# Kernel optimization log

Measured on AMD Instinct MI355X. Metric: run time of the kernel, lower is better.

Reference implementation:

```python
import jax, jax.numpy as jnp
from jax import lax
import numpy as np

D_IN, D, H, W, POOL = 1280, 100, 20, 3, 9
K_SIG, X0 = 1.0, 0.0
EPS = 1e-5


def setup_inputs() -> dict:
    key = jax.random.key(0)
    ks = jax.random.split(key, 8)
    N1, N2 = 512, 512
    return {
        "x1": jax.random.normal(ks[0], (N1, D_IN), jnp.float32),
        "x2": jax.random.normal(ks[1], (N2, D_IN), jnp.float32),
        "W1": jax.random.normal(ks[2], (D, D_IN), jnp.float32) * 0.02,
        "b1": jnp.zeros((D,), jnp.float32),
        "W2": jax.random.normal(ks[3], (H, 2 * D), jnp.float32) * 0.05,
        "b2": jnp.zeros((H,), jnp.float32),
        "bn1_g": jnp.ones((H,), jnp.float32),
        "bn1_b": jnp.zeros((H,), jnp.float32),
        "conv_w": jax.random.normal(ks[4], (1, H, 2 * W + 1, 2 * W + 1), jnp.float32) * 0.05,
        "conv_b": jnp.zeros((1,), jnp.float32),
        "bn2_g": jnp.ones((1,), jnp.float32),
        "bn2_b": jnp.zeros((1,), jnp.float32),
        "gamma": jnp.zeros((1,), jnp.float32),
    }


def reference(x1, x2, W1, b1, W2, b2, bn1_g, bn1_b, conv_w, conv_b, bn2_g, bn2_b, gamma):
    N1, N2 = x1.shape[0], x2.shape[0]
    # fc1 projection (relu1/dropout1 are defined but unused in the original forward)
    a = (x1 @ W1.T + b1)[None]          # [1, N1, D]
    c = (x2 @ W1.T + b2 * 0 + b1)[None] if False else (x2 @ W1.T + b1)[None]  # [1, N2, D]
    # broadcast pairwise |diff| and product -> [1, N1, N2, 2D]
    diff = jnp.abs(a[:, :, None, :] - c[:, None, :, :])
    mul = a[:, :, None, :] * c[:, None, :, :]
    m = jnp.concatenate([diff, mul], axis=-1).reshape(-1, 2 * D)  # [N1*N2, 2D]
    # fc2
    m = m @ W2.T + b2                    # [N1*N2, H]
    # BatchNorm1d in training mode: batch statistics, biased variance
    mu = m.mean(axis=0)
    var = m.var(axis=0)
    m = (m - mu) * lax.rsqrt(var + EPS) * bn1_g + bn1_b
    m = jax.nn.relu(m)
    m = m.reshape(1, N1, N2, H).transpose(0, 3, 1, 2)  # NCHW [1, H, N1, N2]
    # 7x7 conv, padding=W
    C = lax.conv_general_dilated(m, conv_w, (1, 1), [(W, W), (W, W)])
    C = C + conv_b.reshape(1, -1, 1, 1)
    # BatchNorm2d (training mode, biased variance over N,H,W per channel)
    mu2 = C.mean(axis=(0, 2, 3), keepdims=True)
    var2 = C.var(axis=(0, 2, 3), keepdims=True)
    C = (C - mu2) * lax.rsqrt(var2 + EPS) * bn2_g.reshape(1, -1, 1, 1) + bn2_b.reshape(1, -1, 1, 1)
    C = jax.nn.sigmoid(C)
    # MaxPool2d(9, padding=4): stride = kernel, -inf padding
    p = POOL // 2
    B = lax.reduce_window(C, -jnp.inf, lax.max, (1, 1, POOL, POOL), (1, 1, POOL, POOL),
                          [(0, 0), (0, 0), (p, p), (p, p)])
    # mean / unbiased std over dims (1, 2) keepdim
    mean = B.mean(axis=(1, 2), keepdims=True)
    std = jnp.sqrt(B.var(axis=(1, 2), keepdims=True, ddof=1) + EPS)
    Q = jax.nn.relu(B - mean - gamma.reshape(()) * std)
    phat = Q.sum() / (jnp.sign(Q).sum() + 1.0)
    phat = jnp.clip(jax.nn.sigmoid(K_SIG * (phat - X0)), 0.0, 1.0)
    return phat, C
```

## Files before the change

### kernel.cpp

```cpp
#include <hip/hip_runtime.h>
#include <hip/hip_bf16.h>
#include <math.h>

#define N1 512
#define N2 512
#define DIN 1280
#define DD 100
#define HH 20
#define NPIX (N1*N2)
#define PB 57

typedef short bf16x8 __attribute__((ext_vector_type(8)));
typedef float f32x4 __attribute__((ext_vector_type(4)));

static constexpr size_t WS_PP    = 0;
static constexpr size_t WS_W1T   = 204800;
static constexpr size_t WS_W2B   = 332800;
static constexpr size_t WS_M     = 336896;
static constexpr size_t WS_PART  = WS_M + 5242880;
static constexpr size_t WS_CRAW  = WS_PART + 1310720;
static constexpr size_t WS_STATS = WS_CRAW + 262144;
static constexpr size_t WS_B     = WS_STATS + 64;

__global__ __launch_bounds__(256) void kP(const float* __restrict__ W1,
                                          const float* __restrict__ W2,
                                          float* __restrict__ w1t,
                                          unsigned short* __restrict__ w2b,
                                          float* __restrict__ stats) {
  const int tid = threadIdx.x;
  if (blockIdx.x >= 160) {
    int idx = (blockIdx.x - 160) * 256 + tid;
    if (blockIdx.x == 160 && tid < 64) stats[tid] = 0.0f;
    if (idx < 224 * 32) {
      int k = idx >> 5, n = idx & 31;
      float v = (n < HH && k < 200) ? W2[n * 200 + k] : 0.0f;
      __hip_bfloat16 b = __float2bfloat16(v);
      w2b[idx] = *reinterpret_cast<unsigned short*>(&b);
    }
    return;
  }
  __shared__ float sT[32][33];
  const int bx = blockIdx.x % 40, by = blockIdx.x / 40;
  const int tx = tid & 31, ty = tid >> 5;
#pragma unroll
  for (int e = 0; e < 4; ++e) {
    int h = by * 32 + ty + e * 8, k = bx * 32 + tx;
    sT[ty + e * 8][tx] = (h < DD) ? W1[(size_t)h * DIN + k] : 0.0f;
  }
  __syncthreads();
#pragma unroll
  for (int e = 0; e < 4; ++e) {
    int k = bx * 32 + ty + e * 8, h = by * 32 + tx;
    if (h < DD) w1t[(size_t)k * DD + h] = sT[tx][ty + e * 8];
  }
}

__global__ __launch_bounds__(256) void kA(const float* __restrict__ x1,
                                          const float* __restrict__ x2,
                                          const float* __restrict__ w1t,
                                          float* __restrict__ pp) {
  const int tid = threadIdx.x;
  const int w  = __builtin_amdgcn_readfirstlane(tid >> 6);
  const int hh = w & 1, kh = w >> 1;
  const int h = hh * 64 + (tid & 63);
  if (h >= DD) return;
  const int r0 = blockIdx.x * 2;
  const float* xb = (r0 < N1) ? (x1 + (size_t)r0 * DIN) : (x2 + (size_t)(r0 - N1) * DIN);
  const float* xr0 = xb + kh * 640;
  const float* xr1 = xb + DIN + kh * 640;
  const float* w1p = w1t + (size_t)kh * 640 * DD + h;
  float a00 = 0.f, a01 = 0.f, a10 = 0.f, a11 = 0.f;
#pragma unroll 8
  for (int k = 0; k < 640; k += 2) {
    float wA = w1p[(size_t)k * DD];
    float wB = w1p[(size_t)(k + 1) * DD];
    float x00 = xr0[k], x01 = xr0[k + 1];
    float x10 = xr1[k], x11 = xr1[k + 1];
    a00 = fmaf(wA, x00, a00); a01 = fmaf(wB, x01, a01);
    a10 = fmaf(wA, x10, a10); a11 = fmaf(wB, x11, a11);
  }
  pp[(size_t)kh * 102400 + (size_t)r0 * DD + h] = a00 + a01;
  pp[(size_t)kh * 102400 + (size_t)(r0 + 1) * DD + h] = a10 + a11;
}

__global__ __launch_bounds__(256, 2) void kB(const float* __restrict__ pp,
                                             const float* __restrict__ b1,
                                             const unsigned short* __restrict__ w2b,
                                             float* __restrict__ m,
                                             float* __restrict__ stats) {
  __shared__ float sA[8][132];
  __shared__ float sC[64][132];
  __shared__ float wred[4][40];
  const int tid = threadIdx.x;
  const int bi = blockIdx.x >> 3, bj = blockIdx.x & 7;
  for (int idx = tid; idx < 72 * 33; idx += 256) {
    int r = idx / 33, d4 = idx % 33;
    float4 v = {0.f, 0.f, 0.f, 0.f};
    if (d4 < 25) {
      size_t row = (r < 8) ? (size_t)(bi * 8 + r) : (size_t)(N1 + bj * 64 + (r - 8));
      const float* base = pp + row * DD;
      float4 a0 = ((const float4*)base)[d4];
      float4 a1 = ((const float4*)(base + 102400))[d4];
      float4 bb = ((const float4*)b1)[d4];
      v.x = a0.x + a1.x + bb.x;
      v.y = a0.y + a1.y + bb.y;
      v.z = a0.z + a1.z + bb.z;
      v.w = a0.w + a1.w + bb.w;
    }
    if (r < 8) *(float4*)&sA[r][4 * d4] = v;
    else       *(float4*)&sC[r - 8][4 * d4] = v;
  }
  __syncthreads();

  const int w    = tid >> 6;
  const int lane = tid & 63;
  const int ln   = lane & 15;
  const int q    = lane >> 4;
  const int jj   = w * 16 + ln;

  bf16x8 af[7][2];
#pragma unroll
  for (int ks = 0; ks < 7; ++ks)
#pragma unroll
    for (int t = 0; t < 2; ++t) {
      bf16x8 v;
#pragma unroll
      for (int e = 0; e < 8; ++e)
        v[e] = (short)w2b[(ks * 32 + q * 8 + e) * 32 + ln + 16 * t];
      af[ks][t] = v;
    }

  int dOf[14];
  bool isP[14];
  float4 cH[14];
#pragma unroll
  for (int hx = 0; hx < 14; ++hx) {
    int kk = (hx >> 1) * 32 + q * 8 + (hx & 1) * 4;
    bool p = kk >= 100;
    isP[hx] = p;
    int d = p ? kk - 100 : kk;
    dOf[hx] = d;
    cH[hx] = *(const float4*)&sC[jj][d];
  }

  float st_s[8], st_q[8];
#pragma unroll
  for (int r = 0; r < 8; ++r) { st_s[r] = 0.f; st_q[r] = 0.f; }

  const int gj = bj * 64 + jj;
#pragma unroll 1
  for (int ii = 0; ii < 8; ++ii) {
    bf16x8 bf[7];
#pragma unroll
    for (int ks = 0; ks < 7; ++ks) {
      float4 a0 = *(const float4*)&sA[ii][dOf[2 * ks]];
      float4 a1 = *(const float4*)&sA[ii][dOf[2 * ks + 1]];
      float4 c0 = cH[2 * ks], c1 = cH[2 * ks + 1];
      float f0 = isP[2*ks]   ? a0.x * c0.x : fabsf(a0.x - c0.x);
      float f1 = isP[2*ks]   ? a0.y * c0.y : fabsf(a0.y - c0.y);
      float f2 = isP[2*ks]   ? a0.z * c0.z : fabsf(a0.z - c0.z);
      float f3 = isP[2*ks]   ? a0.w * c0.w : fabsf(a0.w - c0.w);
      float f4 = isP[2*ks+1] ? a1.x * c1.x : fabsf(a1.x - c1.x);
      float f5 = isP[2*ks+1] ? a1.y * c1.y : fabsf(a1.y - c1.y);
      float f6 = isP[2*ks+1] ? a1.z * c1.z : fabsf(a1.z - c1.z);
      float f7 = isP[2*ks+1] ? a1.w * c1.w : fabsf(a1.w - c1.w);
      union { bf16x8 v; __hip_bfloat162 h2[4]; } u;
      u.h2[0] = __float22bfloat162_rn(make_float2(f0, f1));
      u.h2[1] = __float22bfloat162_rn(make_float2(f2, f3));
      u.h2[2] = __float22bfloat162_rn(make_float2(f4, f5));
      u.h2[3] = __float22bfloat162_rn(make_float2(f6, f7));
      bf[ks] = u.v;
    }
    f32x4 acc0 = {0.f, 0.f, 0.f, 0.f}, acc1 = {0.f, 0.f, 0.f, 0.f};
#pragma unroll
    for (int ks = 0; ks < 7; ++ks) {
      acc0 = __builtin_amdgcn_mfma_f32_16x16x32_bf16(af[ks][0], bf[ks], acc0, 0, 0, 0);
      acc1 = __builtin_amdgcn_mfma_f32_16x16x32_bf16(af[ks][1], bf[ks], acc1, 0, 0, 0);
    }
    const size_t pix = (size_t)(bi * 8 + ii) * N2 + gj;
#pragma unroll
    for (int r = 0; r < 4; ++r) {
      m[(size_t)(4 * q + r) * NPIX + pix] = acc0[r];
      st_s[r] += acc0[r];
      st_q[r] += acc0[r] * acc0[r];
    }
    if (q == 0) {
#pragma unroll
      for (int r = 0; r < 4; ++r)
        m[(size_t)(16 + r) * NPIX + pix] = acc1[r];
    }
#pragma unroll
    for (int r = 0; r < 4; ++r) {
      st_s[4 + r] += acc1[r];
      st_q[4 + r] += acc1[r] * acc1[r];
    }
  }
#pragma unroll
  for (int r = 0; r < 8; ++r) {
#pragma unroll
    for (int off = 1; off < 16; off <<= 1) {
      st_s[r] += __shfl_xor(st_s[r], off);
      st_q[r] += __shfl_xor(st_q[r], off);
    }
  }
  if (ln == 0) {
#pragma unroll
    for (int r = 0; r < 4; ++r) {
      wred[w][4 * q + r]      = st_s[r];
      wred[w][20 + 4 * q + r] = st_q[r];
    }
    if (q == 0) {
#pragma unroll
      for (int r = 0; r < 4; ++r) {
        wred[w][16 + r] = st_s[4 + r];
        wred[w][36 + r] = st_q[4 + r];
      }
    }
  }
  __syncthreads();
  if (tid < 40)
    atomicAdd(&stats[tid], wred[0][tid] + wred[1][tid] + wred[2][tid] + wred[3][tid]);
}

__global__ __launch_bounds__(256, 4) void kD(const float* __restrict__ m,
                                             const float* __restrict__ bn1g,
                                             const float* __restrict__ bn1b,
                                             const float* __restrict__ cw,
                                             const float* __restrict__ stats,
                                             float* __restrict__ part) {
  __shared__ float sIn[4][38][40];
  __shared__ float sSc[4], sSh[4];
  const int tid = threadIdx.x;
  const int cs = blockIdx.y;
  if (tid < 4) {
    int ch = cs * 4 + tid;
    float s = stats[ch], q = stats[HH + ch];
    float mu = s * (1.0f / NPIX);
    float var = q * (1.0f / NPIX) - mu * mu;
    float g = bn1g[ch] / sqrtf(var + 1e-5f);
    sSc[tid] = g;
    sSh[tid] = bn1b[ch] - mu * g;
  }
  __syncthreads();
  const int by = (blockIdx.x >> 4) * 32, bx = (blockIdx.x & 15) * 32;
  for (int idx = tid; idx < 4 * 38 * 40; idx += 256) {
    int ch4 = idx / 1520, rem = idx % 1520;
    int r = rem / 40, c = rem % 40;
    int gy = by + r - 3, gx = bx + c - 4;
    float v = 0.0f;
    if (gy >= 0 && gy < N1 && gx >= 0 && gx < N2)
      v = fmaxf(m[(size_t)(cs * 4 + ch4) * NPIX + (size_t)gy * N2 + gx] * sSc[ch4] + sSh[ch4], 0.0f);
    sIn[ch4][r][c] = v;
  }
  __syncthreads();
  const int ty = tid >> 4, tx = tid & 15;
  float acc00 = 0.f, acc01 = 0.f, acc10 = 0.f, acc11 = 0.f;
#pragma unroll 1
  for (int ch4 = 0; ch4 < 4; ++ch4) {
    float2 wv[8][5];
#pragma unroll
    for (int rr = 0; rr < 8; ++rr)
#pragma unroll
      for (int qq = 0; qq < 5; ++qq)
        wv[rr][qq] = *(const float2*)&sIn[ch4][2 * ty + rr][2 * tx + 2 * qq];
    const float* wch = cw + (cs * 4 + ch4) * 49;
#pragma unroll
    for (int ky = 0; ky < 7; ++ky)
#pragma unroll
      for (int kx = 0; kx < 7; ++kx) {
        float wt = wch[ky * 7 + kx];
        float e0 = ((kx + 1) & 1) ? wv[ky][(kx + 1) >> 1].y : wv[ky][(kx + 1) >> 1].x;
        float e1 = ((kx + 2) & 1) ? wv[ky][(kx + 2) >> 1].y : wv[ky][(kx + 2) >> 1].x;
        float f0 = ((kx + 1) & 1) ? wv[ky + 1][(kx + 1) >> 1].y : wv[ky + 1][(kx + 1) >> 1].x;
        float f1 = ((kx + 2) & 1) ? wv[ky + 1][(kx + 2) >> 1].y : wv[ky + 1][(kx + 2) >> 1].x;
        acc00 = fmaf(e0, wt, acc00);
        acc01 = fmaf(e1, wt, acc01);
        acc10 = fmaf(f0, wt, acc10);
        acc11 = fmaf(f1, wt, acc11);
      }
  }
  const int oy = by + 2 * ty, ox = bx + 2 * tx;
  float2 r0 = {acc00, acc01}, r1 = {acc10, acc11};
  float* dst = part + (size_t)cs * NPIX;
  *(float2*)&dst[(size_t)oy * N2 + ox] = r0;
  *(float2*)&dst[(size_t)(oy + 1) * N2 + ox] = r1;
}

__global__ __launch_bounds__(256) void kE1(const float* __restrict__ part,
                                           float* __restrict__ stats,
                                           float* __restrict__ Craw) {
  __shared__ float wred[4][2];
  const int i = blockIdx.x * 256 + threadIdx.x;
  float s5 = part[i] + part[NPIX + i] + part[2 * NPIX + i] + part[3 * NPIX + i] + part[4 * NPIX + i];
  Craw[i] = s5;
  float s = s5, q = s5 * s5;
  const int lane = threadIdx.x & 63, wv = threadIdx.x >> 6;
#pragma unroll
  for (int off = 32; off; off >>= 1) {
    s += __shfl_xor(s, off);
    q += __shfl_xor(q, off);
  }
  if (lane == 0) { wred[wv][0] = s; wred[wv][1] = q; }
  __syncthreads();
  if (threadIdx.x < 2) {
    float v = wred[0][threadIdx.x] + wred[1][threadIdx.x] + wred[2][threadIdx.x] + wred[3][threadIdx.x];
    atomicAdd(&stats[2 * HH + threadIdx.x], v);
  }
}

__global__ __launch_bounds__(256) void kE2M(const float* __restrict__ Craw,
                                            const float* __restrict__ stats,
                                            const float* __restrict__ bn2g,
                                            const float* __restrict__ bn2b,
                                            float* __restrict__ Cout,
                                            float* __restrict__ B) {
  const int w = blockIdx.x * 4 + (threadIdx.x >> 6);
  const int lane = threadIdx.x & 63;
  float s = stats[2 * HH], q = stats[2 * HH + 1];
  float mu = s * (1.0f / NPIX);
  float var = q * (1.0f / NPIX) - mu * mu;
  float g = bn2g[0] / sqrtf(var + 1e-5f);
  float b = bn2b[0] - mu * g;
  if (w >= PB * PB) return;
  const int wy = w / PB, wx = w % PB;
  const int y0 = wy * 9 - 4, x0 = wx * 9 - 4;
  float mx = -1e30f;
  for (int e = lane; e < 144; e += 64) {
    int dy = e / 12, dx = e % 12;
    int y = y0 + dy, x = x0 + dx;
    bool inWin = (dy < 9) && (dx < 9);
    bool claim = (y >= 0) && (y < N1) && (x >= 0) && (x < N2) &&
                 (dy < 9 || wy == PB - 1) && (dx < 9 || wx == PB - 1);
    if (claim) {
      float z = Craw[(size_t)y * N2 + x] * g + b;
      float sg = 1.0f / (1.0f + expf(-z));
      Cout[(size_t)y * N2 + x] = sg;
      if (inWin) mx = fmaxf(mx, sg);
    }
  }
#pragma unroll
  for (int off = 32; off; off >>= 1) mx = fmaxf(mx, __shfl_xor(mx, off));
  if (lane == 0) B[w] = mx;
}

__global__ __launch_bounds__(256) void kF(const float* __restrict__ B,
                                          const float* __restrict__ gamma,
                                          float* __restrict__ out0) {
  __shared__ float sB[PB * PB];
  __shared__ float cm[PB], cs[PB];
  __shared__ float r1[4], r2[4];
  const int tid = threadIdx.x;
  for (int i = tid; i < PB * PB; i += 256) sB[i] = B[i];
  __syncthreads();
  if (tid < PB) {
    float s = 0.0f;
    for (int h = 0; h < PB; ++h) s += sB[h * PB + tid];
    float mean = s / (float)PB;
    float v = 0.0f;
    for (int h = 0; h < PB; ++h) { float d = sB[h * PB + tid] - mean; v += d * d; }
    cm[tid] = mean;
    cs[tid] = sqrtf(v / (float)(PB - 1) + 1e-5f);
  }
  __syncthreads();
  const float g = gamma[0];
  float sq = 0.0f, cnt = 0.0f;
  for (int i = tid; i < PB * PB; i += 256) {
    int w = i % PB;
    float qv = sB[i] - cm[w] - g * cs[w];
    if (qv > 0.0f) { sq += qv; cnt += 1.0f; }
  }
#pragma unroll
  for (int off = 32; off; off >>= 1) {
    sq += __shfl_xor(sq, off);
    cnt += __shfl_xor(cnt, off);
  }
  if ((tid & 63) == 0) { r1[tid >> 6] = sq; r2[tid >> 6] = cnt; }
  __syncthreads();
  if (tid == 0) {
    float S = r1[0] + r1[1] + r1[2] + r1[3];
    float Cn = r2[0] + r2[1] + r2[2] + r2[3];
    float phat = S / (Cn + 1.0f);
    float sig = 1.0f / (1.0f + expf(-phat));
    out0[0] = fminf(fmaxf(sig, 0.0f), 1.0f);
  }
}

extern "C" void kernel_launch(void* const* d_in, const int* in_sizes, int n_in,
                              void* d_out, int out_size, void* d_ws, size_t ws_size,
                              hipStream_t stream) {
  const float* x1    = (const float*)d_in[0];
  const float* x2    = (const float*)d_in[1];
  const float* W1    = (const float*)d_in[2];
  const float* b1    = (const float*)d_in[3];
  const float* W2    = (const float*)d_in[4];
  const float* bn1g  = (const float*)d_in[6];
  const float* bn1b  = (const float*)d_in[7];
  const float* convw = (const float*)d_in[8];
  const float* bn2g  = (const float*)d_in[10];
  const float* bn2b  = (const float*)d_in[11];
  const float* gamma = (const float*)d_in[12];

  float* ws    = (float*)d_ws;
  float* pp    = ws + WS_PP;
  float* w1t   = ws + WS_W1T;
  unsigned short* w2b = (unsigned short*)(ws + WS_W2B);
  float* m     = ws + WS_M;
  float* part  = ws + WS_PART;
  float* Craw  = ws + WS_CRAW;
  float* stats = ws + WS_STATS;
  float* Bp    = ws + WS_B;
  float* out   = (float*)d_out;

  kP<<<188, 256, 0, stream>>>(W1, W2, w1t, w2b, stats);
  kA<<<512, 256, 0, stream>>>(x1, x2, w1t, pp);
  kB<<<512, 256, 0, stream>>>(pp, b1, w2b, m, stats);
  kD<<<dim3(256, 5), 256, 0, stream>>>(m, bn1g, bn1b, convw, stats, part);
  kE1<<<1024, 256, 0, stream>>>(part, stats, Craw);
  kE2M<<<(PB * PB + 3) / 4, 256, 0, stream>>>(Craw, stats, bn2g, bn2b, out + 1, Bp);
  kF<<<1, 256, 0, stream>>>(Bp, gamma, out);
}
```

Measured before the change: 102.1 us.

## Fuse conv channel-group reduction into one kernel with double-buffered LDS staging

The 7x7 conv kernel now loops over all 20 channels inside one block instead of splitting channel groups across grid.y. It stages the next four channels from global memory into registers while computing on the current LDS buffer, then writes the final sum straight to Craw and accumulates the BN2 statistics. This removes the partial-sum buffer and the separate kE1 reduction kernel. The cost is only 256 blocks with launch bounds set to 1, so occupancy drops. kA and kF are also reshaped to use larger blocks.

Result: faster. 92.99 us (-8.9%).

```diff
diff --git a/kernel.cpp b/kernel.cpp
--- a/kernel.cpp
+++ b/kernel.cpp
@@ -17,8 +17,7 @@
 static constexpr size_t WS_W1T   = 204800;
 static constexpr size_t WS_W2B   = 332800;
 static constexpr size_t WS_M     = 336896;
-static constexpr size_t WS_PART  = WS_M + 5242880;
-static constexpr size_t WS_CRAW  = WS_PART + 1310720;
+static constexpr size_t WS_CRAW  = WS_M + 5242880;
 static constexpr size_t WS_STATS = WS_CRAW + 262144;
 static constexpr size_t WS_B     = WS_STATS + 64;
 
@@ -55,16 +54,18 @@
   }
 }
 
-__global__ __launch_bounds__(256) void kA(const float* __restrict__ x1,
+__global__ __launch_bounds__(512) void kA(const float* __restrict__ x1,
                                           const float* __restrict__ x2,
                                           const float* __restrict__ w1t,
                                           float* __restrict__ pp) {
   const int tid = threadIdx.x;
   const int w  = __builtin_amdgcn_readfirstlane(tid >> 6);
-  const int hh = w & 1, kh = w >> 1;
+  const int rp = w >> 1, hh = w & 1;
   const int h = hh * 64 + (tid & 63);
   if (h >= DD) return;
-  const int r0 = blockIdx.x * 2;
+  const int kh = blockIdx.x & 1;
+  const int rb = (blockIdx.x >> 1) * 8;
+  const int r0 = rb + rp * 2;
   const float* xb = (r0 < N1) ? (x1 + (size_t)r0 * DIN) : (x2 + (size_t)(r0 - N1) * DIN);
   const float* xr0 = xb + kh * 640;
   const float* xr1 = xb + DIN + kh * 640;
@@ -222,89 +223,114 @@
     atomicAdd(&stats[tid], wred[0][tid] + wred[1][tid] + wred[2][tid] + wred[3][tid]);
 }
 
-__global__ __launch_bounds__(256, 4) void kD(const float* __restrict__ m,
+__global__ __launch_bounds__(256, 1) void kD(const float* __restrict__ m,
                                              const float* __restrict__ bn1g,
                                              const float* __restrict__ bn1b,
                                              const float* __restrict__ cw,
-                                             const float* __restrict__ stats,
-                                             float* __restrict__ part) {
-  __shared__ float sIn[4][38][40];
-  __shared__ float sSc[4], sSh[4];
+                                             float* __restrict__ stats,
+                                             float* __restrict__ Craw) {
+  __shared__ float sIn[2][4][38][40];
+  __shared__ float sSc[HH], sSh[HH];
+  __shared__ float wsum[4][2];
   const int tid = threadIdx.x;
-  const int cs = blockIdx.y;
-  if (tid < 4) {
-    int ch = cs * 4 + tid;
-    float s = stats[ch], q = stats[HH + ch];
+  if (tid < HH) {
+    float s = stats[tid], q = stats[HH + tid];
     float mu = s * (1.0f / NPIX);
     float var = q * (1.0f / NPIX) - mu * mu;
-    float g = bn1g[ch] / sqrtf(var + 1e-5f);
+    float g = bn1g[tid] / sqrtf(var + 1e-5f);
     sSc[tid] = g;
-    sSh[tid] = bn1b[ch] - mu * g;
-  }
-  __syncthreads();
+    sSh[tid] = bn1b[tid] - mu * g;
+  }
   const int by = (blockIdx.x >> 4) * 32, bx = (blockIdx.x & 15) * 32;
-  for (int idx = tid; idx < 4 * 38 * 40; idx += 256) {
-    int ch4 = idx / 1520, rem = idx % 1520;
-    int r = rem / 40, c = rem % 40;
-    int gy = by + r - 3, gx = bx + c - 4;
-    float v = 0.0f;
-    if (gy >= 0 && gy < N1 && gx >= 0 && gx < N2)
-      v = fmaxf(m[(size_t)(cs * 4 + ch4) * NPIX + (size_t)gy * N2 + gx] * sSc[ch4] + sSh[ch4], 0.0f);
-    sIn[ch4][r][c] = v;
+  const int w = tid >> 6, lane = tid & 63;
+  const int gxs = bx + lane - 4;
+  const bool colOk = (lane < 40) && (gxs >= 0) && (gxs < N2);
+  float ld[38];
+  {
+    const float* mp = m + (size_t)w * NPIX + gxs;
+#pragma unroll
+    for (int r = 0; r < 38; ++r) {
+      int gy = by + r - 3;
+      ld[r] = (colOk && gy >= 0 && gy < N1) ? mp[(size_t)gy * N2] : 0.0f;
+    }
+  }
+  __syncthreads();
+  if (lane < 40) {
+    float sc = sSc[w], sh = sSh[w];
+#pragma unroll
+    for (int r = 0; r < 38; ++r) {
+      int gy = by + r - 3;
+      bool ok = colOk && gy >= 0 && gy < N1;
+      sIn[0][w][r][lane] = ok ? fmaxf(fmaf(ld[r], sc, sh), 0.0f) : 0.0f;
+    }
   }
   __syncthreads();
   const int ty = tid >> 4, tx = tid & 15;
   float acc00 = 0.f, acc01 = 0.f, acc10 = 0.f, acc11 = 0.f;
 #pragma unroll 1
-  for (int ch4 = 0; ch4 < 4; ++ch4) {
-    float2 wv[8][5];
-#pragma unroll
-    for (int rr = 0; rr < 8; ++rr)
-#pragma unroll
-      for (int qq = 0; qq < 5; ++qq)
-        wv[rr][qq] = *(const float2*)&sIn[ch4][2 * ty + rr][2 * tx + 2 * qq];
-    const float* wch = cw + (cs * 4 + ch4) * 49;
-#pragma unroll
-    for (int ky = 0; ky < 7; ++ky)
-#pragma unroll
-      for (int kx = 0; kx < 7; ++kx) {
-        float wt = wch[ky * 7 + kx];
-        float e0 = ((kx + 1) & 1) ? wv[ky][(kx + 1) >> 1].y : wv[ky][(kx + 1) >> 1].x;
-        float e1 = ((kx + 2) & 1) ? wv[ky][(kx + 2) >> 1].y : wv[ky][(kx + 2) >> 1].x;
-        float f0 = ((kx + 1) & 1) ? wv[ky + 1][(kx + 1) >> 1].y : wv[ky + 1][(kx + 1) >> 1].x;
-        float f1 = ((kx + 2) & 1) ? wv[ky + 1][(kx + 2) >> 1].y : wv[ky + 1][(kx + 2) >> 1].x;
-        acc00 = fmaf(e0, wt, acc00);
-        acc01 = fmaf(e1, wt, acc01);
-        acc10 = fmaf(f0, wt, acc10);
-        acc11 = fmaf(f1, wt, acc11);
+  for (int cc = 0; cc < 5; ++cc) {
+    if (cc < 4) {
+      const float* mp = m + (size_t)((cc + 1) * 4 + w) * NPIX + gxs;
+#pragma unroll
+      for (int r = 0; r < 38; ++r) {
+        int gy = by + r - 3;
+        ld[r] = (colOk && gy >= 0 && gy < N1) ? mp[(size_t)gy * N2] : 0.0f;
       }
+    }
+    const int cur = cc & 1;
+#pragma unroll 1
+    for (int ch4 = 0; ch4 < 4; ++ch4) {
+      float2 win[8][5];
+#pragma unroll
+      for (int rr = 0; rr < 8; ++rr)
+#pragma unroll
+        for (int qq = 0; qq < 5; ++qq)
+          win[rr][qq] = *(const float2*)&sIn[cur][ch4][2 * ty + rr][2 * tx + 2 * qq];
+      const float* wch = cw + (cc * 4 + ch4) * 49;
+#pragma unroll
+      for (int ky = 0; ky < 7; ++ky)
+#pragma unroll
+        for (int kx = 0; kx < 7; ++kx) {
+          float wt = wch[ky * 7 + kx];
+          float e0 = ((kx + 1) & 1) ? win[ky][(kx + 1) >> 1].y : win[ky][(kx + 1) >> 1].x;
+          float e1 = ((kx + 2) & 1) ? win[ky][(kx + 2) >> 1].y : win[ky][(kx + 2) >> 1].x;
+          float f0 = ((kx + 1) & 1) ? win[ky + 1][(kx + 1) >> 1].y : win[ky + 1][(kx + 1) >> 1].x;
+          float f1 = ((kx + 2) & 1) ? win[ky + 1][(kx + 2) >> 1].y : win[ky + 1][(kx + 2) >> 1].x;
+          acc00 = fmaf(e0, wt, acc00);
+          acc01 = fmaf(e1, wt, acc01);
+          acc10 = fmaf(f0, wt, acc10);
+          acc11 = fmaf(f1, wt, acc11);
+        }
+    }
+    __syncthreads();
+    if (cc < 4 && lane < 40) {
+      int ch = (cc + 1) * 4 + w;
+      float sc = sSc[ch], sh = sSh[ch];
+#pragma unroll
+      for (int r = 0; r < 38; ++r) {
+        int gy = by + r - 3;
+        bool ok = colOk && gy >= 0 && gy < N1;
+        sIn[cur ^ 1][w][r][lane] = ok ? fmaxf(fmaf(ld[r], sc, sh), 0.0f) : 0.0f;
+      }
+    }
+    __syncthreads();
   }
   const int oy = by + 2 * ty, ox = bx + 2 * tx;
   float2 r0 = {acc00, acc01}, r1 = {acc10, acc11};
-  float* dst = part + (size_t)cs * NPIX;
-  *(float2*)&dst[(size_t)oy * N2 + ox] = r0;
-  *(float2*)&dst[(size_t)(oy + 1) * N2 + ox] = r1;
-}
-
-__global__ __launch_bounds__(256) void kE1(const float* __restrict__ part,
-                                           float* __restrict__ stats,
-                                           float* __restrict__ Craw) {
-  __shared__ float wred[4][2];
-  const int i = blockIdx.x * 256 + threadIdx.x;
-  float s5 = part[i] + part[NPIX + i] + part[2 * NPIX + i] + part[3 * NPIX + i] + part[4 * NPIX + i];
-  Craw[i] = s5;
-  float s = s5, q = s5 * s5;
-  const int lane = threadIdx.x & 63, wv = threadIdx.x >> 6;
+  *(float2*)&Craw[(size_t)oy * N2 + ox] = r0;
+  *(float2*)&Craw[(size_t)(oy + 1) * N2 + ox] = r1;
+  float s = acc00 + acc01 + acc10 + acc11;
+  float q = acc00 * acc00 + acc01 * acc01 + acc10 * acc10 + acc11 * acc11;
 #pragma unroll
   for (int off = 32; off; off >>= 1) {
     s += __shfl_xor(s, off);
     q += __shfl_xor(q, off);
   }
-  if (lane == 0) { wred[wv][0] = s; wred[wv][1] = q; }
-  __syncthreads();
-  if (threadIdx.x < 2) {
-    float v = wred[0][threadIdx.x] + wred[1][threadIdx.x] + wred[2][threadIdx.x] + wred[3][threadIdx.x];
-    atomicAdd(&stats[2 * HH + threadIdx.x], v);
+  if (lane == 0) { wsum[w][0] = s; wsum[w][1] = q; }
+  __syncthreads();
+  if (tid < 2) {
+    float v = wsum[0][tid] + wsum[1][tid] + wsum[2][tid] + wsum[3][tid];
+    atomicAdd(&stats[2 * HH + tid], v);
   }
 }
 
@@ -343,28 +369,35 @@
   if (lane == 0) B[w] = mx;
 }
 
-__global__ __launch_bounds__(256) void kF(const float* __restrict__ B,
-                                          const float* __restrict__ gamma,
-                                          float* __restrict__ out0) {
+__global__ __launch_bounds__(1024) void kF(const float* __restrict__ B,
+                                           const float* __restrict__ gamma,
+                                           float* __restrict__ out0) {
   __shared__ float sB[PB * PB];
   __shared__ float cm[PB], cs[PB];
-  __shared__ float r1[4], r2[4];
+  __shared__ float r1[16], r2[16];
   const int tid = threadIdx.x;
-  for (int i = tid; i < PB * PB; i += 256) sB[i] = B[i];
-  __syncthreads();
-  if (tid < PB) {
+  for (int i = tid; i < PB * PB; i += 1024) sB[i] = B[i];
+  __syncthreads();
+  if (tid < PB * 16) {
+    int c = tid >> 4, g = tid & 15;
     float s = 0.0f;
-    for (int h = 0; h < PB; ++h) s += sB[h * PB + tid];
+    for (int h = g; h < PB; h += 16) s += sB[h * PB + c];
+#pragma unroll
+    for (int off = 1; off < 16; off <<= 1) s += __shfl_xor(s, off);
     float mean = s / (float)PB;
     float v = 0.0f;
-    for (int h = 0; h < PB; ++h) { float d = sB[h * PB + tid] - mean; v += d * d; }
-    cm[tid] = mean;
-    cs[tid] = sqrtf(v / (float)(PB - 1) + 1e-5f);
+    for (int h = g; h < PB; h += 16) { float d = sB[h * PB + c] - mean; v += d * d; }
+#pragma unroll
+    for (int off = 1; off < 16; off <<= 1) v += __shfl_xor(v, off);
+    if (g == 0) {
+      cm[c] = mean;
+      cs[c] = sqrtf(v / (float)(PB - 1) + 1e-5f);
+    }
   }
   __syncthreads();
   const float g = gamma[0];
   float sq = 0.0f, cnt = 0.0f;
-  for (int i = tid; i < PB * PB; i += 256) {
+  for (int i = tid; i < PB * PB; i += 1024) {
     int w = i % PB;
     float qv = sB[i] - cm[w] - g * cs[w];
     if (qv > 0.0f) { sq += qv; cnt += 1.0f; }
@@ -377,8 +410,9 @@
   if ((tid & 63) == 0) { r1[tid >> 6] = sq; r2[tid >> 6] = cnt; }
   __syncthreads();
   if (tid == 0) {
-    float S = r1[0] + r1[1] + r1[2] + r1[3];
-    float Cn = r2[0] + r2[1] + r2[2] + r2[3];
+    float S = 0.f, Cn = 0.f;
+#pragma unroll
+    for (int e = 0; e < 16; ++e) { S += r1[e]; Cn += r2[e]; }
     float phat = S / (Cn + 1.0f);
     float sig = 1.0f / (1.0f + expf(-phat));
     out0[0] = fminf(fmaxf(sig, 0.0f), 1.0f);
@@ -405,17 +439,15 @@
   float* w1t   = ws + WS_W1T;
   unsigned short* w2b = (unsigned short*)(ws + WS_W2B);
   float* m     = ws + WS_M;
-  float* part  = ws + WS_PART;
   float* Craw  = ws + WS_CRAW;
   float* stats = ws + WS_STATS;
   float* Bp    = ws + WS_B;
   float* out   = (float*)d_out;
 
   kP<<<188, 256, 0, stream>>>(W1, W2, w1t, w2b, stats);
-  kA<<<512, 256, 0, stream>>>(x1, x2, w1t, pp);
+  kA<<<256, 512, 0, stream>>>(x1, x2, w1t, pp);
   kB<<<512, 256, 0, stream>>>(pp, b1, w2b, m, stats);
-  kD<<<dim3(256, 5), 256, 0, stream>>>(m, bn1g, bn1b, convw, stats, part);
-  kE1<<<1024, 256, 0, stream>>>(part, stats, Craw);
+  kD<<<256, 256, 0, stream>>>(m, bn1g, bn1b, convw, stats, Craw);
   kE2M<<<(PB * PB + 3) / 4, 256, 0, stream>>>(Craw, stats, bn2g, bn2b, out + 1, Bp);
-  kF<<<1, 256, 0, stream>>>(Bp, gamma, out);
-}
+  kF<<<1, 1024, 0, stream>>>(Bp, gamma, out);
+}
```
